# Kernel optimization log

Hardware: AMD Instinct MI355X
Metric: run time of the kernel (lower is better)

## Reference

```python
import jax, jax.numpy as jnp
import numpy as np

N, T = 2048, 128
E, H = 128, 256
V, L = 30000, 1000


def setup_inputs() -> dict:
    key = jax.random.key(0)
    ks = jax.random.split(key, 10)
    tokens = jax.random.randint(ks[0], (N, T), 0, V)
    lengths = jax.random.randint(ks[1], (N,), 1, T + 1)  # each seq has >=1 valid step
    labels = jax.random.randint(ks[2], (N,), 0, L)
    s_e = 1.0 / np.sqrt(H)
    emb = jax.random.normal(ks[3], (V, E), dtype=jnp.float32)
    W_ih = jax.random.uniform(ks[4], (4 * H, E), minval=-s_e, maxval=s_e, dtype=jnp.float32)
    W_hh = jax.random.uniform(ks[5], (4 * H, H), minval=-s_e, maxval=s_e, dtype=jnp.float32)
    b_ih = jax.random.uniform(ks[6], (4 * H,), minval=-s_e, maxval=s_e, dtype=jnp.float32)
    b_hh = jax.random.uniform(ks[7], (4 * H,), minval=-s_e, maxval=s_e, dtype=jnp.float32)
    s_h = 1.0 / np.sqrt(H)
    W_out = jax.random.uniform(ks[8], (L, H), minval=-s_h, maxval=s_h, dtype=jnp.float32)
    b_out = jax.random.uniform(ks[9], (L,), minval=-s_h, maxval=s_h, dtype=jnp.float32)
    return {"tokens": tokens, "lengths": lengths, "labels": labels, "emb": emb,
            "W_ih": W_ih, "W_hh": W_hh, "b_ih": b_ih, "b_hh": b_hh,
            "W_out": W_out, "b_out": b_out}


def _lstm_final(tokens, lengths, emb, W_ih, W_hh, b_ih, b_hh):
    # Batched ragged LSTM: freeze state once t >= length (matches per-seq loop).
    x = emb[tokens]                                    # [N,T,E]
    xg = jnp.einsum('nte,ge->ntg', x, W_ih) + b_ih     # [N,T,4H] precomputed input gates
    xg_t = jnp.transpose(xg, (1, 0, 2))                # [T,N,4H]
    mask_t = (jnp.arange(T)[:, None] < lengths[None, :])  # [T,N]
    h0 = jnp.zeros((tokens.shape[0], H), jnp.float32)
    c0 = jnp.zeros_like(h0)

    def step(carry, inp):
        h, c = carry
        xgt, m = inp
        gates = xgt + h @ W_hh.T + b_hh                # [N,4H]
        i, f, g, o = jnp.split(gates, 4, axis=-1)
        i = jax.nn.sigmoid(i); f = jax.nn.sigmoid(f)
        g = jnp.tanh(g); o = jax.nn.sigmoid(o)
        c_new = f * c + i * g
        h_new = o * jnp.tanh(c_new)
        mm = m[:, None]
        return (jnp.where(mm, h_new, h), jnp.where(mm, c_new, c)), None

    (h_f, c_f), _ = jax.lax.scan(step, (h0, c0), (xg_t, mask_t))
    return h_f, c_f                                    # final valid h, c per sequence


def reference(tokens, lengths, labels, emb, W_ih, W_hh, b_ih, b_hh, W_out, b_out):
    h_f, c_f = _lstm_final(tokens, lengths, emb, W_ih, W_hh, b_ih, b_hh)
    logits = h_f @ W_out.T + b_out                     # [N,L]
    logp = jax.nn.log_softmax(logits, axis=-1)
    # NLLLoss per sequence, summed then divided by count -> mean
    loss = -jnp.mean(logp[jnp.arange(logp.shape[0]), labels])
    embeds = jnp.mean(c_f, axis=0)                     # mean of final cell states, [H]
    return embeds, loss
```

## Files before the change

### kernel.cpp

```cpp
#include <hip/hip_runtime.h>
#include <hip/hip_bf16.h>
#include <math.h>

#define NSEQ 2048
#define TT   128
#define EE   128
#define HH   256
#define GG   1024
#define LL   1000
#define NT   512
#define NGRP 32
#define NMEM 8
#define SEQG 64
#define NKT  12
#define NMT  64
#define NKT_O 8
#define WSA_ELEMS (NMT * NKT * 64 * 8)
#define WSO_ELEMS (NMT * NKT_O * 64 * 8)
#define GHF_SHORTS ((size_t)NGRP * NMEM * 2 * 4 * 64 * 8)

typedef __attribute__((ext_vector_type(8))) short bf16x8;
typedef __attribute__((ext_vector_type(4))) float f32x4;
typedef unsigned long long u64;

__device__ __forceinline__ unsigned short f2bf(float f) {
    union { float f; unsigned u; } v; v.f = f;
    unsigned r = v.u + 0x7FFF + ((v.u >> 16) & 1);
    return (unsigned short)(r >> 16);
}
__device__ __forceinline__ float sigf(float x) { return 1.0f / (1.0f + __expf(-x)); }
__device__ __forceinline__ float tanh_fast(float x) { return 1.0f - 2.0f / (1.0f + __expf(2.0f * x)); }

__device__ __forceinline__ void st8_sys(unsigned short* p, unsigned lo, unsigned hi) {
    u64 v = (u64)lo | ((u64)hi << 32);
    __hip_atomic_store((u64*)p, v, __ATOMIC_RELAXED, __HIP_MEMORY_SCOPE_SYSTEM);
}
__device__ __forceinline__ bf16x8 ld16_sys(const unsigned short* p) {
    u64 lo = __hip_atomic_load((const u64*)p,       __ATOMIC_RELAXED, __HIP_MEMORY_SCOPE_SYSTEM);
    u64 hi = __hip_atomic_load((const u64*)(p + 4), __ATOMIC_RELAXED, __HIP_MEMORY_SCOPE_SYSTEM);
    union { u64 q[2]; bf16x8 v; } u; u.q[0] = lo; u.q[1] = hi;
    return u.v;
}

__global__ void init_out_kernel(float* out, int* flags) {
    int i = blockIdx.x * blockDim.x + threadIdx.x;
    if (i < HH + 1) out[i] = 0.0f;
    if (i < NGRP * NMEM) flags[i] = 0;
}

__global__ void convert_weights(const float* __restrict__ Wih, const float* __restrict__ Whh,
                                const float* __restrict__ Wout,
                                unsigned short* __restrict__ wsA, unsigned short* __restrict__ wsO) {
    int gid = blockIdx.x * blockDim.x + threadIdx.x;
    if (gid < NMT * NKT * 64) {
        int lane = gid & 63, tile = gid >> 6;
        int kt = tile % NKT, mt = tile / NKT;
        int row = mt * 16 + (lane & 15);
        int kb  = kt * 32 + (lane >> 4) * 8;
        unsigned short o[8];
#pragma unroll
        for (int j = 0; j < 8; ++j) {
            int k = kb + j;
            float v = (k < EE) ? Wih[row * EE + k] : Whh[row * HH + (k - EE)];
            o[j] = f2bf(v);
        }
        uint4 pk;
        pk.x = o[0] | ((unsigned)o[1] << 16); pk.y = o[2] | ((unsigned)o[3] << 16);
        pk.z = o[4] | ((unsigned)o[5] << 16); pk.w = o[6] | ((unsigned)o[7] << 16);
        *(uint4*)(wsA + (size_t)gid * 8) = pk;
    } else {
        int g2 = gid - NMT * NKT * 64;
        if (g2 < NMT * NKT_O * 64) {
            int lane = g2 & 63, tile = g2 >> 6;
            int kt = tile % NKT_O, mt = tile / NKT_O;
            int row = mt * 16 + (lane & 15);
            int ub  = kt * 32 + (lane >> 4) * 8;
            unsigned short o[8];
#pragma unroll
            for (int j = 0; j < 8; ++j)
                o[j] = (row < LL) ? f2bf(Wout[row * HH + ub + j]) : (unsigned short)0;
            uint4 pk;
            pk.x = o[0] | ((unsigned)o[1] << 16); pk.y = o[2] | ((unsigned)o[3] << 16);
            pk.z = o[4] | ((unsigned)o[5] << 16); pk.w = o[6] | ((unsigned)o[7] << 16);
            *(uint4*)(wsO + (size_t)g2 * 8) = pk;
        }
    }
}

__launch_bounds__(NT, 2)
__global__ void lstm_group_kernel(
    const int* __restrict__ tokens, const int* __restrict__ lengths,
    const int* __restrict__ labels, const float* __restrict__ emb,
    const float* __restrict__ bih,  const float* __restrict__ bhh,
    const float* __restrict__ bout,
    const unsigned short* __restrict__ wsA, const unsigned short* __restrict__ wsO,
    unsigned short* __restrict__ ghf, int* __restrict__ flags,
    float* __restrict__ out)
{
    __shared__ __align__(16) unsigned short wlds[8 * 12 * 64 * 8];
    __shared__ __align__(16) unsigned short xfS[4 * 4 * 64 * 8];
    __shared__ __align__(16) unsigned short hf[2 * 4 * 64 * 8];
    __shared__ float redm[8][16];
    __shared__ float reds[8][16];
    __shared__ int   labv[SEQG];
    __shared__ int   ready_s;

    const int tid = threadIdx.x;
    const int w   = tid >> 6;
    const int l   = tid & 63;
    const int lq  = l >> 4;
    const int ls  = l & 15;
    const int jj  = w >> 2;
    const int cg  = w & 3;
    const int grp = blockIdx.x & (NGRP - 1);
    const int m   = blockIdx.x >> 5;
    const int n0  = grp * SEQG;

    int* const flagBase = flags + grp * NMEM;

    int maxlen = lengths[n0 + l];
#pragma unroll
    for (int s = 1; s < 64; s <<= 1) maxlen = max(maxlen, __shfl_xor(maxlen, s, 64));
    const int len_s = lengths[n0 + cg * 16 + ls];

    if (tid < SEQG) labv[tid] = labels[n0 + tid];
    if (tid == 0) ready_s = 0;

    f32x4 biasv[4];
#pragma unroll
    for (int g = 0; g < 4; ++g)
#pragma unroll
        for (int r = 0; r < 4; ++r) {
            int row = 256 * g + 32 * m + 16 * jj + 4 * lq + r;
            biasv[g][r] = bih[row] + bhh[row];
        }

    for (int idx = tid; idx < 8 * 12 * 64; idx += NT) {
        int mtl = idx / 768;
        int rem = idx - mtl * 768;
        int kt = rem >> 6, l2 = rem & 63;
        int g = mtl >> 1, j2 = mtl & 1;
        int gmt = 16 * g + 2 * m + j2;
        *(uint4*)&wlds[(size_t)idx * 8] =
            *(const uint4*)(wsA + ((size_t)(gmt * NKT + kt) * 64 + l2) * 8);
    }

    if (tid < 256) {
        uint4 z = {0, 0, 0, 0};
        *(uint4*)&hf[(size_t)tid * 8] = z;
        size_t base = ((size_t)((grp * NMEM + m) * 2 + 0) * 4) * 512 + (size_t)tid * 8;
        st8_sys(&ghf[base], 0, 0);
        st8_sys(&ghf[base + 4], 0, 0);
    }

    const int xs_s   = tid & 63;
    const int xs_oct = tid >> 6;

    auto stageX = [&](const f32x4* xv) {
#pragma unroll
        for (int dc = 0; dc < 4; ++dc) {
            int d0 = 16 * xs_oct + 4 * dc;
            int kt = d0 >> 5, cgs = xs_s >> 4;
            int lanep = (xs_s & 15) + 16 * ((d0 >> 3) & 3);
            uint2 pk;
            pk.x = f2bf(xv[dc][0]) | ((unsigned)f2bf(xv[dc][1]) << 16);
            pk.y = f2bf(xv[dc][2]) | ((unsigned)f2bf(xv[dc][3]) << 16);
            *(uint2*)&xfS[(size_t)((kt * 4 + cgs) * 64 + lanep) * 8 + (d0 & 4)] = pk;
        }
    };

    {
        int tok = tokens[(n0 + xs_s) * TT + 0];
        const float* er = emb + (size_t)tok * EE + 16 * xs_oct;
        f32x4 x0[4];
#pragma unroll
        for (int dc = 0; dc < 4; ++dc) x0[dc] = *(const f32x4*)(er + 4 * dc);
        stageX(x0);
    }
    __syncthreads();
    if (tid == 0)
        __hip_atomic_store(&flagBase[m], 1, __ATOMIC_RELAXED, __HIP_MEMORY_SCOPE_SYSTEM);

    f32x4 xv[4];
    if (maxlen > 1) {
        int tok = tokens[(n0 + xs_s) * TT + 1];
        const float* er = emb + (size_t)tok * EE + 16 * xs_oct;
#pragma unroll
        for (int dc = 0; dc < 4; ++dc) xv[dc] = *(const f32x4*)(er + 4 * dc);
    }

    f32x4 acc[4], accN[4];
#pragma unroll
    for (int g = 0; g < 4; ++g) acc[g] = biasv[g];
#pragma unroll
    for (int kt = 0; kt < 4; ++kt) {
        const bf16x8 bx = *(const bf16x8*)&xfS[(size_t)((kt * 4 + cg) * 64 + l) * 8];
#pragma unroll
        for (int g = 0; g < 4; ++g)
            acc[g] = __builtin_amdgcn_mfma_f32_16x16x32_bf16(
                *(const bf16x8*)&wlds[(size_t)(((2 * g + jj) * 12 + kt) * 64 + l) * 8],
                bx, acc[g], 0, 0, 0);
    }
    __syncthreads();

    auto relay_wait = [&](int need) {
        if (w == 0) {
            int f;
            do {
                f = 0x7fffffff;
                if (l < NMEM)
                    f = __hip_atomic_load(&flagBase[l], __ATOMIC_RELAXED, __HIP_MEMORY_SCOPE_SYSTEM);
                f = min(f, __shfl_xor(f, 1, 64));
                f = min(f, __shfl_xor(f, 2, 64));
                f = min(f, __shfl_xor(f, 4, 64));
                f = __shfl(f, 0, 64);
                if (f < need) __builtin_amdgcn_s_sleep(2);
            } while (f < need);
            __hip_atomic_store(&ready_s, need, __ATOMIC_RELEASE, __HIP_MEMORY_SCOPE_WORKGROUP);
        } else {
            while (__hip_atomic_load(&ready_s, __ATOMIC_ACQUIRE, __HIP_MEMORY_SCOPE_WORKGROUP) < need)
                __builtin_amdgcn_s_sleep(1);
        }
    };

    float c_reg[4], h_reg[4];
#pragma unroll
    for (int r = 0; r < 4; ++r) { c_reg[r] = 0.0f; h_reg[r] = 0.0f; }

    const int u8      = 2 * jj + (lq >> 1);
    const int lanep_h = 16 * u8 + ls;
    const int joff_h  = 4 * (lq & 1);
    const size_t gb0  = ((size_t)((grp * NMEM + m) * 2 + 0) * 4 + cg) * 512 + (size_t)lanep_h * 8 + joff_h;
    const size_t gb1  = gb0 + 4 * 512;

    for (int t = 0; t < maxlen; ++t) {
        const int cur = t & 1, nxt = cur ^ 1;
        const bool doX = (t + 1 < maxlen);

        if (doX) stageX(xv);
        const bf16x8 bo = *(const bf16x8*)&hf[(size_t)((cur * 4 + cg) * 64 + l) * 8];
        if (doX) __syncthreads();

        if (t + 2 < maxlen) {
            int tok = tokens[(n0 + xs_s) * TT + t + 2];
            const float* er = emb + (size_t)tok * EE + 16 * xs_oct;
#pragma unroll
            for (int dc = 0; dc < 4; ++dc) xv[dc] = *(const f32x4*)(er + 4 * dc);
        }

        if (doX) {
#pragma unroll
            for (int g = 0; g < 4; ++g) accN[g] = biasv[g];
#pragma unroll
            for (int kt = 0; kt < 4; ++kt) {
                const bf16x8 bx = *(const bf16x8*)&xfS[(size_t)((kt * 4 + cg) * 64 + l) * 8];
#pragma unroll
                for (int g = 0; g < 4; ++g)
                    accN[g] = __builtin_amdgcn_mfma_f32_16x16x32_bf16(
                        *(const bf16x8*)&wlds[(size_t)(((2 * g + jj) * 12 + kt) * 64 + l) * 8],
                        bx, accN[g], 0, 0, 0);
            }
        }

        relay_wait(t + 1);

        bf16x8 bp[7];
#pragma unroll
        for (int i = 0; i < 7; ++i) {
            int p = i + (i >= m ? 1 : 0);
            size_t b = ((size_t)((grp * NMEM + p) * 2 + cur) * 4 + cg) * 512;
            bp[i] = ld16_sys(&ghf[b + (size_t)l * 8]);
        }

#pragma unroll
        for (int g = 0; g < 4; ++g)
            acc[g] = __builtin_amdgcn_mfma_f32_16x16x32_bf16(
                *(const bf16x8*)&wlds[(size_t)(((2 * g + jj) * 12 + 4 + m) * 64 + l) * 8],
                bo, acc[g], 0, 0, 0);
#pragma unroll
        for (int i = 0; i < 7; ++i) {
            int p = i + (i >= m ? 1 : 0);
            int kt = 4 + p;
#pragma unroll
            for (int g = 0; g < 4; ++g)
                acc[g] = __builtin_amdgcn_mfma_f32_16x16x32_bf16(
                    *(const bf16x8*)&wlds[(size_t)(((2 * g + jj) * 12 + kt) * 64 + l) * 8],
                    bp[i], acc[g], 0, 0, 0);
        }

        const bool live = (t < len_s);
#pragma unroll
        for (int r = 0; r < 4; ++r) {
            if (live) {
                float ig = sigf(acc[0][r]);
                float fg = sigf(acc[1][r]);
                float gg = tanh_fast(acc[2][r]);
                float og = sigf(acc[3][r]);
                float cc = fg * c_reg[r] + ig * gg;
                c_reg[r] = cc;
                h_reg[r] = og * tanh_fast(cc);
            }
        }

        if (doX) {
#pragma unroll
            for (int g = 0; g < 4; ++g) acc[g] = accN[g];
        }

        {
            uint2 hp;
            hp.x = f2bf(h_reg[0]) | ((unsigned)f2bf(h_reg[1]) << 16);
            hp.y = f2bf(h_reg[2]) | ((unsigned)f2bf(h_reg[3]) << 16);
            *(uint2*)&hf[(size_t)((nxt * 4 + cg) * 64 + lanep_h) * 8 + joff_h] = hp;
            st8_sys(&ghf[((t + 1) & 1) ? gb1 : gb0], hp.x, hp.y);
        }

        __syncthreads();
        if (tid == 0)
            __hip_atomic_store(&flagBase[m], t + 2, __ATOMIC_RELAXED, __HIP_MEMORY_SCOPE_SYSTEM);
    }

#pragma unroll
    for (int r = 0; r < 4; ++r) {
        float v = c_reg[r];
        v += __shfl_xor(v, 1, 64);
        v += __shfl_xor(v, 2, 64);
        v += __shfl_xor(v, 4, 64);
        v += __shfl_xor(v, 8, 64);
        if (ls == 0)
            atomicAdd(&out[32 * m + 16 * jj + 4 * lq + r], v * (1.0f / NSEQ));
    }

    if (m == 0) {
        relay_wait(maxlen + 1);
        const int fin = maxlen & 1;
        float* lg = (float*)wlds;
        float lossAcc = 0.0f;

        for (int cgo = 0; cgo < 4; ++cgo) {
            bf16x8 bq[8];
#pragma unroll
            for (int p = 0; p < 8; ++p) {
                size_t b = ((size_t)((grp * NMEM + p) * 2 + fin) * 4 + cgo) * 512;
                bq[p] = ld16_sys(&ghf[b + (size_t)l * 8]);
            }
            __syncthreads();
#pragma unroll
            for (int i = 0; i < 8; ++i) {
                int mt = 8 * w + i;
                f32x4 a = {0.0f, 0.0f, 0.0f, 0.0f};
#pragma unroll
                for (int p = 0; p < 8; ++p)
                    a = __builtin_amdgcn_mfma_f32_16x16x32_bf16(
                        *(const bf16x8*)(wsO + ((size_t)(mt * NKT_O + p) * 64 + l) * 8),
                        bq[p], a, 0, 0, 0);
#pragma unroll
                for (int r = 0; r < 4; ++r) {
                    int cls = 16 * mt + 4 * lq + r;
                    lg[(size_t)ls * 1024 + cls] = (cls < LL) ? (a[r] + bout[cls]) : -INFINITY;
                }
            }
            __syncthreads();
            const int s2 = tid >> 5;
            const int i2 = tid & 31;
            const float* row = &lg[(size_t)s2 * 1024];
            float mx = -INFINITY;
#pragma unroll
            for (int k = 0; k < 32; ++k) mx = fmaxf(mx, row[i2 + 32 * k]);
            mx = fmaxf(mx, __shfl_xor(mx, 1, 64));
            mx = fmaxf(mx, __shfl_xor(mx, 2, 64));
            mx = fmaxf(mx, __shfl_xor(mx, 4, 64));
            mx = fmaxf(mx, __shfl_xor(mx, 8, 64));
            mx = fmaxf(mx, __shfl_xor(mx, 16, 64));
            float sm = 0.0f;
#pragma unroll
            for (int k = 0; k < 32; ++k) sm += __expf(row[i2 + 32 * k] - mx);
            sm += __shfl_xor(sm, 1, 64);
            sm += __shfl_xor(sm, 2, 64);
            sm += __shfl_xor(sm, 4, 64);
            sm += __shfl_xor(sm, 8, 64);
            sm += __shfl_xor(sm, 16, 64);
            if (i2 == 0) {
                int lab = labv[cgo * 16 + s2];
                float lp = row[lab] - mx - __logf(sm);
                lossAcc += -lp;
            }
        }
        if ((tid & 31) == 0)
            atomicAdd(&out[HH], lossAcc * (1.0f / NSEQ));
    }
}

extern "C" void kernel_launch(void* const* d_in, const int* in_sizes, int n_in,
                              void* d_out, int out_size, void* d_ws, size_t ws_size,
                              hipStream_t stream)
{
    const int*   tokens  = (const int*)d_in[0];
    const int*   lengths = (const int*)d_in[1];
    const int*   labels  = (const int*)d_in[2];
    const float* emb     = (const float*)d_in[3];
    const float* Wih     = (const float*)d_in[4];
    const float* Whh     = (const float*)d_in[5];
    const float* bih     = (const float*)d_in[6];
    const float* bhh     = (const float*)d_in[7];
    const float* Wout    = (const float*)d_in[8];
    const float* bout    = (const float*)d_in[9];
    float* out = (float*)d_out;

    unsigned short* wsA  = (unsigned short*)d_ws;
    unsigned short* wsO  = wsA + WSA_ELEMS;
    unsigned short* ghf  = wsO + WSO_ELEMS;
    int*            flg  = (int*)(ghf + GHF_SHORTS);

    hipLaunchKernelGGL(init_out_kernel, dim3(1), dim3(512), 0, stream, out, flg);
    {
        int nthr = NMT * NKT * 64 + NMT * NKT_O * 64;
        hipLaunchKernelGGL(convert_weights, dim3((nthr + 255) / 256), dim3(256), 0, stream,
                           Wih, Whh, Wout, wsA, wsO);
    }
    hipLaunchKernelGGL(lstm_group_kernel, dim3(NGRP * NMEM), dim3(NT), 0, stream,
                       tokens, lengths, labels, emb, bih, bhh, bout, wsA, wsO, ghf, flg, out);
}
```

Before: 700.7 us.

## Stage peer hidden-state tiles through LDS with one wave per peer

Waves 0-6 now each fetch one peer member's full hidden-state tile from global memory with system-scope loads and write it to a new shared buffer. After a workgroup barrier, all waves read their slices from LDS for the recurrent MFMAs. Before, every wave loaded all seven peer slices itself, and waves sharing a column group issued duplicate global loads. This cuts duplicated coherent global traffic per step, at the cost of an extra __syncthreads and an LDS round trip on the serial critical path. Launch bounds are also relaxed to one block per SIMD group, allowing more registers per thread.

```diff
diff --git a/kernel.cpp b/kernel.cpp
--- a/kernel.cpp
+++ b/kernel.cpp
@@ -35,14 +35,18 @@
     u64 v = (u64)lo | ((u64)hi << 32);
     __hip_atomic_store((u64*)p, v, __ATOMIC_RELAXED, __HIP_MEMORY_SCOPE_SYSTEM);
 }
-__device__ __forceinline__ bf16x8 ld16_sys(const unsigned short* p) {
+__device__ __forceinline__ uint4 ld16_sys_u(const unsigned short* p) {
     u64 lo = __hip_atomic_load((const u64*)p,       __ATOMIC_RELAXED, __HIP_MEMORY_SCOPE_SYSTEM);
     u64 hi = __hip_atomic_load((const u64*)(p + 4), __ATOMIC_RELAXED, __HIP_MEMORY_SCOPE_SYSTEM);
-    union { u64 q[2]; bf16x8 v; } u; u.q[0] = lo; u.q[1] = hi;
+    union { u64 q[2]; uint4 v; } u; u.q[0] = lo; u.q[1] = hi;
     return u.v;
 }
-
-__global__ void init_out_kernel(float* out, int* flags) {
+__device__ __forceinline__ bf16x8 ld16_sys(const unsigned short* p) {
+    union { uint4 q; bf16x8 v; } u; u.q = ld16_sys_u(p);
+    return u.v;
+}
+
+__global__ void init_all_kernel(float* out, int* flags) {
     int i = blockIdx.x * blockDim.x + threadIdx.x;
     if (i < HH + 1) out[i] = 0.0f;
     if (i < NGRP * NMEM) flags[i] = 0;
@@ -87,7 +91,7 @@
     }
 }
 
-__launch_bounds__(NT, 2)
+__launch_bounds__(NT, 1)
 __global__ void lstm_group_kernel(
     const int* __restrict__ tokens, const int* __restrict__ lengths,
     const int* __restrict__ labels, const float* __restrict__ emb,
@@ -100,8 +104,7 @@
     __shared__ __align__(16) unsigned short wlds[8 * 12 * 64 * 8];
     __shared__ __align__(16) unsigned short xfS[4 * 4 * 64 * 8];
     __shared__ __align__(16) unsigned short hf[2 * 4 * 64 * 8];
-    __shared__ float redm[8][16];
-    __shared__ float reds[8][16];
+    __shared__ __align__(16) unsigned short pbuf[7 * 4 * 64 * 8];
     __shared__ int   labv[SEQG];
     __shared__ int   ready_s;
 
@@ -221,6 +224,7 @@
             while (__hip_atomic_load(&ready_s, __ATOMIC_ACQUIRE, __HIP_MEMORY_SCOPE_WORKGROUP) < need)
                 __builtin_amdgcn_s_sleep(1);
         }
+        asm volatile("" ::: "memory");
     };
 
     float c_reg[4], h_reg[4];
@@ -233,6 +237,8 @@
     const size_t gb0  = ((size_t)((grp * NMEM + m) * 2 + 0) * 4 + cg) * 512 + (size_t)lanep_h * 8 + joff_h;
     const size_t gb1  = gb0 + 4 * 512;
 
+    const int pw = (w < 7) ? (w + (w >= m ? 1 : 0)) : 0;
+
     for (int t = 0; t < maxlen; ++t) {
         const int cur = t & 1, nxt = cur ^ 1;
         const bool doX = (t + 1 < maxlen);
@@ -264,12 +270,12 @@
 
         relay_wait(t + 1);
 
-        bf16x8 bp[7];
-#pragma unroll
-        for (int i = 0; i < 7; ++i) {
-            int p = i + (i >= m ? 1 : 0);
-            size_t b = ((size_t)((grp * NMEM + p) * 2 + cur) * 4 + cg) * 512;
-            bp[i] = ld16_sys(&ghf[b + (size_t)l * 8]);
+        uint4 ptile[4];
+        if (w < 7) {
+            const unsigned short* src = ghf + ((size_t)((grp * NMEM + pw) * 2 + cur) * 2048);
+#pragma unroll
+            for (int k = 0; k < 4; ++k)
+                ptile[k] = ld16_sys_u(src + (size_t)(l + 64 * k) * 8);
         }
 
 #pragma unroll
@@ -277,15 +283,23 @@
             acc[g] = __builtin_amdgcn_mfma_f32_16x16x32_bf16(
                 *(const bf16x8*)&wlds[(size_t)(((2 * g + jj) * 12 + 4 + m) * 64 + l) * 8],
                 bo, acc[g], 0, 0, 0);
+
+        if (w < 7) {
+#pragma unroll
+            for (int k = 0; k < 4; ++k)
+                *(uint4*)&pbuf[((size_t)w * 256 + l + 64 * k) * 8] = ptile[k];
+        }
+        __syncthreads();
+
 #pragma unroll
         for (int i = 0; i < 7; ++i) {
             int p = i + (i >= m ? 1 : 0);
-            int kt = 4 + p;
+            const bf16x8 bp = *(const bf16x8*)&pbuf[((size_t)i * 256 + cg * 64 + l) * 8];
 #pragma unroll
             for (int g = 0; g < 4; ++g)
                 acc[g] = __builtin_amdgcn_mfma_f32_16x16x32_bf16(
-                    *(const bf16x8*)&wlds[(size_t)(((2 * g + jj) * 12 + kt) * 64 + l) * 8],
-                    bp[i], acc[g], 0, 0, 0);
+                    *(const bf16x8*)&wlds[(size_t)(((2 * g + jj) * 12 + 4 + p) * 64 + l) * 8],
+                    bp, acc[g], 0, 0, 0);
         }
 
         const bool live = (t < len_s);
@@ -412,7 +426,7 @@
     unsigned short* ghf  = wsO + WSO_ELEMS;
     int*            flg  = (int*)(ghf + GHF_SHORTS);
 
-    hipLaunchKernelGGL(init_out_kernel, dim3(1), dim3(512), 0, stream, out, flg);
+    hipLaunchKernelGGL(init_all_kernel, dim3(1), dim3(512), 0, stream, out, flg);
     {
         int nthr = NMT * NKT * 64 + NMT * NKT_O * 64;
         hipLaunchKernelGGL(convert_weights, dim3((nthr + 255) / 256), dim3(256), 0, stream,
```

New measurement: 726.3 us. 3.7% more time.
